# Performance work log

Hardware: AMD Instinct MI355X
Metric: run time of the kernel (lower is better)

## Reference

```python
import jax, jax.numpy as jnp
import numpy as np

N = 50000      # nodes
E = 800000     # edges
IN = 256       # in_dim
H = 3          # num_heads
C = 64         # hidden_dim (per head)
D = H * C      # per-layer width = 192
OUT = 64       # out_dim
EPS_BN = 1e-5


def _gat_layer(h, W, att_src, att_dst, bias, src, dst):
    """PyG GATConv (concat=True, no self loops, eval/no dropout).
    h: [N, F_in], W: [F_in, H*C], att_src/att_dst: [H, C], bias: [H*C]."""
    x = (h @ W).reshape(-1, H, C)                       # [N, H, C]
    a_s = jnp.einsum('nhc,hc->nh', x, att_src)          # [N, H]
    a_d = jnp.einsum('nhc,hc->nh', x, att_dst)          # [N, H]
    e = jax.nn.leaky_relu(a_s[src] + a_d[dst], 0.2)     # [E, H]
    # segment softmax over incoming edges of each destination node
    m = jax.ops.segment_max(e, dst, num_segments=N)     # [N, H]
    m = jnp.where(jnp.isfinite(m), m, 0.0)
    w = jnp.exp(e - m[dst])                             # [E, H]
    den = jax.ops.segment_sum(w, dst, num_segments=N)   # [N, H]
    alpha = w / (den[dst] + 1e-16)                      # [E, H]
    out = jax.ops.segment_sum(x[src] * alpha[:, :, None], dst, num_segments=N)
    return out.reshape(-1, D) + bias                    # [N, H*C]


def _batchnorm(h, gamma, beta):
    mu = h.mean(0)
    var = h.var(0)
    return (h - mu) * jax.lax.rsqrt(var + EPS_BN) * gamma + beta


def setup_inputs() -> dict:
    key = jax.random.key(0)
    ks = jax.random.split(key, 16)
    s_in = 1.0 / np.sqrt(IN)
    s_d = 1.0 / np.sqrt(D)
    inp = {
        'x': jax.random.normal(ks[0], (N, IN), jnp.float32),
        'W1': jax.random.normal(ks[1], (IN, D), jnp.float32) * s_in,
        'att_src1': jax.random.normal(ks[2], (H, C), jnp.float32) * s_d,
        'att_dst1': jax.random.normal(ks[3], (H, C), jnp.float32) * s_d,
        'b1': jnp.zeros((D,), jnp.float32),
        'g1': jnp.ones((D,), jnp.float32),
        'beta1': jnp.zeros((D,), jnp.float32),
        'W2': jax.random.normal(ks[4], (D, D), jnp.float32) * s_d,
        'att_src2': jax.random.normal(ks[5], (H, C), jnp.float32) * s_d,
        'att_dst2': jax.random.normal(ks[6], (H, C), jnp.float32) * s_d,
        'b2': jnp.zeros((D,), jnp.float32),
        'g2': jnp.ones((D,), jnp.float32),
        'beta2': jnp.zeros((D,), jnp.float32),
        'Wf': jax.random.normal(ks[7], (D, OUT), jnp.float32) * s_d,
        'bf': jnp.zeros((OUT,), jnp.float32),
        'edge_index': jax.random.randint(ks[8], (2, E), 0, N, jnp.int64),
    }
    return inp


def reference(x, W1, att_src1, att_dst1, b1, g1, beta1,
              W2, att_src2, att_dst2, b2, g2, beta2,
              Wf, bf, edge_index):
    src, dst = edge_index[0], edge_index[1]
    h1 = _gat_layer(x, W1, att_src1, att_dst1, b1, src, dst)
    h1 = _batchnorm(jax.nn.relu(h1), g1, beta1)
    h2 = _gat_layer(h1, W2, att_src2, att_dst2, b2, src, dst)
    h2 = _batchnorm(jax.nn.relu(h2), g2, beta2)
    h_sum = h1 + h2
    return h_sum @ Wf + bf
```

## Files before the change

kernel.cpp:

```cpp
#include <hip/hip_runtime.h>

#define NN 50000
#define NE 800000
#define DIN 256
#define NH 3
#define HC 64
#define DD 192
#define DF 64
#define NB 196

typedef __attribute__((ext_vector_type(8))) short s8bf;
typedef __attribute__((ext_vector_type(8))) unsigned short u16x8;
typedef __attribute__((ext_vector_type(4))) float f32x4;

__device__ __forceinline__ unsigned short f2bf(float f) {
    unsigned u = __float_as_uint(f);
    unsigned r = u + 0x7fffu + ((u >> 16) & 1u);
    return (unsigned short)(r >> 16);
}
__device__ __forceinline__ float bf2f(unsigned short h) {
    return __uint_as_float(((unsigned)h) << 16);
}
__device__ __forceinline__ void split2(float f, unsigned short& h, unsigned short& l) {
    h = f2bf(f);
    l = f2bf(f - bf2f(h));
}
__device__ __forceinline__ float rl_f(float v, int j) {
    return __int_as_float(__builtin_amdgcn_readlane(__float_as_int(v), j));
}

#define W1G (DIN / 8 * DD)
#define W2G (DD / 8 * DD)
#define WFG (DD / 8 * DF)
__global__ __launch_bounds__(256)
void wsplit_all(const float* __restrict__ W1, const float* __restrict__ W2,
                const float* __restrict__ Wf,
                unsigned short* __restrict__ W1hT, unsigned short* __restrict__ W1lT,
                unsigned short* __restrict__ W2hT, unsigned short* __restrict__ W2lT,
                unsigned short* __restrict__ WfhT, unsigned short* __restrict__ WflT) {
    int idx = blockIdx.x * 256 + threadIdx.x;
    const float* W; unsigned short *Wh, *Wl; int K, D, base;
    if (idx < W1G)                  { W = W1; Wh = W1hT; Wl = W1lT; K = DIN; D = DD; base = idx; }
    else if (idx < W1G + W2G)       { W = W2; Wh = W2hT; Wl = W2lT; K = DD;  D = DD; base = idx - W1G; }
    else if (idx < W1G + W2G + WFG) { W = Wf; Wh = WfhT; Wl = WflT; K = DD;  D = DF; base = idx - W1G - W2G; }
    else return;
    int kb = base / D, d = base - kb * D;
    u16x8 hv, lv;
#pragma unroll
    for (int q = 0; q < 8; ++q) {
        unsigned short h, l;
        split2(W[(size_t)(kb * 8 + q) * D + d], h, l);
        hv[q] = h; lv[q] = l;
    }
    *(u16x8*)(Wh + (size_t)d * K + kb * 8) = hv;
    *(u16x8*)(Wl + (size_t)d * K + kb * 8) = lv;
}

__global__ void bn_fin(const float* __restrict__ s1, const float* __restrict__ s2,
                       const float* __restrict__ g, const float* __restrict__ beta,
                       float* __restrict__ scale, float* __restrict__ shift) {
    int j = threadIdx.x;
    const float invn = 1.0f / NN;
    float mu = s1[j] * invn;
    float var = s2[j] * invn - mu * mu;
    float sc = g[j] * rsqrtf(var + 1e-5f);
    scale[j] = sc;
    shift[j] = beta[j] - mu * sc;
}

template<int K, int DOUT, int MODE, bool DOTS>
__global__ __launch_bounds__(256)
void mfma_gemm(const float* __restrict__ A1, const float* __restrict__ A2,
               const float* __restrict__ bb1, const float* __restrict__ sc1,
               const float* __restrict__ sh1,
               const float* __restrict__ bb2, const float* __restrict__ sc2,
               const float* __restrict__ sh2,
               const unsigned short* __restrict__ BhT, const unsigned short* __restrict__ BlT,
               const float* __restrict__ att_s, const float* __restrict__ att_d,
               float4* __restrict__ as4o, float4* __restrict__ ad4o,
               const float* __restrict__ obias, float* __restrict__ Yf,
               unsigned short* __restrict__ Yb, int n) {
    constexpr int NT = DOUT / 64;
    __shared__ unsigned short AH[2][512][8];
    __shared__ float sdots[DOTS ? 4 : 1][64][6];

    const int tid = threadIdx.x;
    const int wave = tid >> 6, lane = tid & 63;
    const int r = lane & 15, kg = lane >> 4;
    const int row0 = blockIdx.x * 64;
    const int col0 = wave * (DOUT / 4);

    auto stage = [&](int buf, int k0) {
#pragma unroll
        for (int half = 0; half < 2; ++half) {
            int slot = tid + half * 256;
            int row = slot >> 3, kb8 = slot & 7;
            int grow = min(row0 + row, n - 1);
            int j = k0 + kb8 * 8;
            const float* ap = A1 + (size_t)grow * K + j;
            float v[8];
            *(float4*)&v[0] = *(const float4*)ap;
            *(float4*)&v[4] = *(const float4*)(ap + 4);
            if constexpr (MODE >= 1) {
#pragma unroll
                for (int q = 0; q < 8; ++q)
                    v[q] = fmaxf(v[q] + bb1[j + q], 0.f) * sc1[j + q] + sh1[j + q];
            }
            if constexpr (MODE == 2) {
                const float* ap2 = A2 + (size_t)grow * K + j;
                float u[8];
                *(float4*)&u[0] = *(const float4*)ap2;
                *(float4*)&u[4] = *(const float4*)(ap2 + 4);
#pragma unroll
                for (int q = 0; q < 8; ++q)
                    v[q] += fmaxf(u[q] + bb2[j + q], 0.f) * sc2[j + q] + sh2[j + q];
            }
            u16x8 hv;
#pragma unroll
            for (int q = 0; q < 8; ++q)
                hv[q] = f2bf(v[q]);
            int sw = (row << 3) | (kb8 ^ (row & 7));
            *(u16x8*)&AH[buf][sw][0] = hv;
        }
    };

    int boff[NT];
#pragma unroll
    for (int t = 0; t < NT; ++t)
        boff[t] = (col0 + t * 16 + r) * K + kg * 8;

    f32x4 acc[4][NT] = {};

    stage(0, 0);
    __syncthreads();

    for (int k0 = 0; k0 < K; k0 += 64) {
        const int buf = (k0 >> 6) & 1;
        if (k0 + 64 < K) stage(buf ^ 1, k0 + 64);
#pragma unroll
        for (int s = 0; s < 2; ++s) {
            s8bf bh[NT], bl[NT];
#pragma unroll
            for (int t = 0; t < NT; ++t) {
                bh[t] = *(const s8bf*)(BhT + boff[t] + k0 + s * 32);
                bl[t] = *(const s8bf*)(BlT + boff[t] + k0 + s * 32);
            }
            s8bf ah[4];
#pragma unroll
            for (int g = 0; g < 4; ++g) {
                int row = g * 16 + r;
                int sw = (row << 3) | ((s * 4 + kg) ^ (row & 7));
                ah[g] = *(const s8bf*)&AH[buf][sw][0];
            }
#pragma unroll
            for (int g = 0; g < 4; ++g)
#pragma unroll
                for (int t = 0; t < NT; ++t) {
                    acc[g][t] = __builtin_amdgcn_mfma_f32_16x16x32_bf16(ah[g], bh[t], acc[g][t], 0, 0, 0);
                    acc[g][t] = __builtin_amdgcn_mfma_f32_16x16x32_bf16(ah[g], bl[t], acc[g][t], 0, 0, 0);
                }
        }
        __syncthreads();
    }

#pragma unroll
    for (int t = 0; t < NT; ++t) {
        int col = col0 + t * 16 + r;
        float b = (MODE == 2) ? obias[col] : 0.f;
#pragma unroll
        for (int g = 0; g < 4; ++g) {
#pragma unroll
            for (int rr = 0; rr < 4; ++rr) {
                int row = row0 + g * 16 + kg * 4 + rr;
                if (row < n) {
                    if constexpr (MODE == 2)
                        Yf[(size_t)row * DOUT + col] = acc[g][t][rr] + b;
                    else
                        Yb[(size_t)row * DOUT + col] = f2bf(acc[g][t][rr]);
                }
            }
        }
    }

    if constexpr (DOTS) {
        float asv[NT], adv[NT];
        int headt[NT];
#pragma unroll
        for (int t = 0; t < NT; ++t) {
            int col = col0 + t * 16 + r;
            asv[t] = att_s[col];
            adv[t] = att_d[col];
            headt[t] = (col0 + t * 16) >> 6;
        }
#pragma unroll
        for (int g = 0; g < 4; ++g) {
#pragma unroll
            for (int rr = 0; rr < 4; ++rr) {
                float rs0 = 0.f, rs1 = 0.f, rs2 = 0.f;
                float rd0 = 0.f, rd1 = 0.f, rd2 = 0.f;
#pragma unroll
                for (int t = 0; t < NT; ++t) {
                    float v = acc[g][t][rr];
                    float s = v * asv[t], dd = v * adv[t];
                    if (headt[t] == 0)      { rs0 += s; rd0 += dd; }
                    else if (headt[t] == 1) { rs1 += s; rd1 += dd; }
                    else                    { rs2 += s; rd2 += dd; }
                }
#pragma unroll
                for (int m = 1; m < 16; m <<= 1) {
                    rs0 += __shfl_xor(rs0, m); rs1 += __shfl_xor(rs1, m); rs2 += __shfl_xor(rs2, m);
                    rd0 += __shfl_xor(rd0, m); rd1 += __shfl_xor(rd1, m); rd2 += __shfl_xor(rd2, m);
                }
                if (r == 0) {
                    int row = g * 16 + kg * 4 + rr;
                    sdots[wave][row][0] = rs0; sdots[wave][row][1] = rs1; sdots[wave][row][2] = rs2;
                    sdots[wave][row][3] = rd0; sdots[wave][row][4] = rd1; sdots[wave][row][5] = rd2;
                }
            }
        }
        __syncthreads();
        if (tid < 64) {
            int row = row0 + tid;
            if (row < n) {
                float s0 = 0.f, s1 = 0.f, s2 = 0.f, d0 = 0.f, d1 = 0.f, d2 = 0.f;
#pragma unroll
                for (int w = 0; w < 4; ++w) {
                    s0 += sdots[w][tid][0]; s1 += sdots[w][tid][1]; s2 += sdots[w][tid][2];
                    d0 += sdots[w][tid][3]; d1 += sdots[w][tid][4]; d2 += sdots[w][tid][5];
                }
                as4o[row] = make_float4(s0, s1, s2, 0.f);
                ad4o[row] = make_float4(d0, d1, d2, 0.f);
            }
        }
    }
}

__global__ void hist_kernel(const int* __restrict__ dst, int* __restrict__ deg, int ne) {
    int e = blockIdx.x * blockDim.x + threadIdx.x;
    if (e < ne) atomicAdd(&deg[dst[e]], 1);
}

__global__ __launch_bounds__(256)
void blocksum_kernel(const int* __restrict__ deg, int* __restrict__ bsum) {
    int i = blockIdx.x * 256 + threadIdx.x;
    int v = (i < NN) ? deg[i] : 0;
#pragma unroll
    for (int off = 32; off; off >>= 1) v += __shfl_down(v, off);
    __shared__ int ws[4];
    if ((threadIdx.x & 63) == 0) ws[threadIdx.x >> 6] = v;
    __syncthreads();
    if (threadIdx.x == 0) bsum[blockIdx.x] = ws[0] + ws[1] + ws[2] + ws[3];
}

__global__ __launch_bounds__(256)
void scan_bsums(const int* __restrict__ bsum, int* __restrict__ boff,
                int* __restrict__ rowptr) {
    __shared__ int s[256];
    int t = threadIdx.x;
    int v = (t < NB) ? bsum[t] : 0;
    s[t] = v;
    __syncthreads();
    for (int off = 1; off < 256; off <<= 1) {
        int u = (t >= off) ? s[t - off] : 0;
        __syncthreads();
        s[t] += u;
        __syncthreads();
    }
    if (t < NB) boff[t] = s[t] - v;
    if (t == 255) rowptr[NN] = s[255];
}

__global__ __launch_bounds__(256)
void expand_kernel(const int* __restrict__ deg, const int* __restrict__ boff,
                   int* __restrict__ rowptr, int* __restrict__ cursor) {
    __shared__ int s[256];
    int t = threadIdx.x;
    int i = blockIdx.x * 256 + t;
    int v = (i < NN) ? deg[i] : 0;
    s[t] = v;
    __syncthreads();
    for (int off = 1; off < 256; off <<= 1) {
        int u = (t >= off) ? s[t - off] : 0;
        __syncthreads();
        s[t] += u;
        __syncthreads();
    }
    if (i < NN) {
        int excl = s[t] - v + boff[blockIdx.x];
        rowptr[i] = excl;
        cursor[i] = excl;
    }
}

__global__ void scatter_kernel(const int* __restrict__ src, const int* __restrict__ dst,
                               int* __restrict__ cursor, int* __restrict__ csr_src, int ne) {
    int e = blockIdx.x * blockDim.x + threadIdx.x;
    if (e >= ne) return;
    int d = dst[e];
    int pos = atomicAdd(&cursor[d], 1);
    csr_src[pos] = src[e];
}

__global__ __launch_bounds__(256)
void gat_gather(const unsigned short* __restrict__ xf,
                const float4* __restrict__ as4, const float4* __restrict__ ad4,
                const int* __restrict__ rowptr, const int* __restrict__ csr_src,
                float* __restrict__ outp) {
    int d = blockIdx.x * 4 + (threadIdx.x >> 6);
    if (d >= NN) return;
    const int lane = threadIdx.x & 63;
    const int beg = rowptr[d], end = rowptr[d + 1];
    const float4 adv = ad4[d];

    float a0 = 0.f, a1 = 0.f, a2 = 0.f;
    float den0 = 0.f, den1 = 0.f, den2 = 0.f;

    for (int base = beg; base < end; base += 64) {
        const int nb = min(64, end - base);
        int sl = 0;
        float w0 = 0.f, w1 = 0.f, w2 = 0.f;
        if (lane < nb) {
            sl = csr_src[base + lane];
            float4 av = as4[sl];
            float e0 = av.x + adv.x;
            float e1 = av.y + adv.y;
            float e2 = av.z + adv.z;
            e0 = e0 > 0.f ? e0 : 0.2f * e0;
            e1 = e1 > 0.f ? e1 : 0.2f * e1;
            e2 = e2 > 0.f ? e2 : 0.2f * e2;
            w0 = __expf(e0); w1 = __expf(e1); w2 = __expf(e2);
        }
        float r0 = w0, r1 = w1, r2 = w2;
#pragma unroll
        for (int off = 1; off < 64; off <<= 1) {
            r0 += __shfl_xor(r0, off);
            r1 += __shfl_xor(r1, off);
            r2 += __shfl_xor(r2, off);
        }
        den0 += r0; den1 += r1; den2 += r2;

        int j = 0;
        for (; j + 8 <= nb; j += 8) {
            const unsigned short* xp[8];
            float uw0[8], uw1[8], uw2[8];
#pragma unroll
            for (int k = 0; k < 8; ++k) {
                int s = __builtin_amdgcn_readlane(sl, j + k);
                xp[k] = xf + (size_t)s * DD;
                uw0[k] = rl_f(w0, j + k);
                uw1[k] = rl_f(w1, j + k);
                uw2[k] = rl_f(w2, j + k);
            }
            unsigned short f0[8], f1[8], f2[8];
#pragma unroll
            for (int k = 0; k < 8; ++k) {
                f0[k] = xp[k][lane];
                f1[k] = xp[k][64 + lane];
                f2[k] = xp[k][128 + lane];
            }
#pragma unroll
            for (int k = 0; k < 8; ++k) {
                a0 = fmaf(bf2f(f0[k]), uw0[k], a0);
                a1 = fmaf(bf2f(f1[k]), uw1[k], a1);
                a2 = fmaf(bf2f(f2[k]), uw2[k], a2);
            }
        }
        for (; j < nb; ++j) {
            int s = __builtin_amdgcn_readlane(sl, j);
            float u0 = rl_f(w0, j), u1 = rl_f(w1, j), u2 = rl_f(w2, j);
            const unsigned short* xp = xf + (size_t)s * DD;
            a0 = fmaf(bf2f(xp[lane]),       u0, a0);
            a1 = fmaf(bf2f(xp[64 + lane]),  u1, a1);
            a2 = fmaf(bf2f(xp[128 + lane]), u2, a2);
        }
    }
    size_t o = (size_t)d * DD + lane;
    outp[o]       = a0 / (den0 + 1e-16f);
    outp[o + 64]  = a1 / (den1 + 1e-16f);
    outp[o + 128] = a2 / (den2 + 1e-16f);
}

__global__ __launch_bounds__(192)
void bn_stats(const float* __restrict__ hbuf, const float* __restrict__ bias,
              float* __restrict__ s1, float* __restrict__ s2, int n) {
    int j = threadIdx.x;
    float b = bias[j];
    int r0 = blockIdx.x * 64;
    int r1 = min(r0 + 64, n);
    float a = 0.f, q = 0.f;
    for (int r = r0; r < r1; ++r) {
        float v = hbuf[(size_t)r * DD + j] + b;
        v = fmaxf(v, 0.f);
        a += v; q += v * v;
    }
    atomicAdd(&s1[j], a);
    atomicAdd(&s2[j], q);
}

extern "C" void kernel_launch(void* const* d_in, const int* in_sizes, int n_in,
                              void* d_out, int out_size, void* d_ws, size_t ws_size,
                              hipStream_t stream) {
    const float* x   = (const float*)d_in[0];
    const float* W1  = (const float*)d_in[1];
    const float* as1 = (const float*)d_in[2];
    const float* ad1 = (const float*)d_in[3];
    const float* b1  = (const float*)d_in[4];
    const float* g1  = (const float*)d_in[5];
    const float* be1 = (const float*)d_in[6];
    const float* W2  = (const float*)d_in[7];
    const float* as2 = (const float*)d_in[8];
    const float* ad2 = (const float*)d_in[9];
    const float* b2  = (const float*)d_in[10];
    const float* g2  = (const float*)d_in[11];
    const float* be2 = (const float*)d_in[12];
    const float* Wf  = (const float*)d_in[13];
    const float* bf  = (const float*)d_in[14];
    const int*   ei  = (const int*)d_in[15];
    const int* src = ei;
    const int* dst = ei + NE;
    float* out = (float*)d_out;

    float* ws = (float*)d_ws;
    float* CB1 = ws;
    float* CB2 = CB1 + (size_t)NN * DD;
    float4* AS4 = (float4*)(CB2 + (size_t)NN * DD);
    float4* AD4 = AS4 + NN;
    int* DEG   = (int*)(AD4 + NN);
    float* S1a = (float*)(DEG + NN);
    float* S2a = S1a + DD;
    float* S1b = S2a + DD;
    float* S2b = S1b + DD;
    float* SC1 = S2b + DD;
    float* SH1 = SC1 + DD;
    float* SC2 = SH1 + DD;
    float* SH2 = SC2 + DD;
    int* ROWPTR = (int*)(SH2 + DD);
    int* CURSOR = ROWPTR + NN + 1;
    int* BSUM   = CURSOR + NN;
    int* BOFF   = BSUM + NB;
    int* CSRS   = BOFF + NB;
    unsigned short* R    = (unsigned short*)(CSRS + NE);
    unsigned short* Abf  = R;
    unsigned short* W1hT = Abf + (size_t)NN * DD;
    unsigned short* W1lT = W1hT + DIN * DD;
    unsigned short* W2hT = W1lT + DIN * DD;
    unsigned short* W2lT = W2hT + DD * DD;
    unsigned short* WfhT = W2lT + DD * DD;
    unsigned short* WflT = WfhT + DD * DF;

    const int edge_grid = (NE + 255) / 256;
    const int gemm_grid = (NN + 63) / 64;
    const int gat_grid  = (NN + 3) / 4;
    const int bns_grid  = (NN + 63) / 64;
    const int wsp_grid  = (W1G + W2G + WFG + 255) / 256;

    hipMemsetAsync(DEG, 0, (size_t)NN * 4 + 4 * DD * 4, stream);

    hist_kernel<<<edge_grid, 256, 0, stream>>>(dst, DEG, NE);
    blocksum_kernel<<<NB, 256, 0, stream>>>(DEG, BSUM);
    scan_bsums<<<1, 256, 0, stream>>>(BSUM, BOFF, ROWPTR);
    expand_kernel<<<NB, 256, 0, stream>>>(DEG, BOFF, ROWPTR, CURSOR);
    scatter_kernel<<<edge_grid, 256, 0, stream>>>(src, dst, CURSOR, CSRS, NE);

    wsplit_all<<<wsp_grid, 256, 0, stream>>>(W1, W2, Wf, W1hT, W1lT, W2hT, W2lT, WfhT, WflT);

    mfma_gemm<DIN, DD, 0, true><<<gemm_grid, 256, 0, stream>>>(
        x, nullptr,
        nullptr, nullptr, nullptr,
        nullptr, nullptr, nullptr,
        W1hT, W1lT, as1, ad1, AS4, AD4, nullptr, nullptr, Abf, NN);
    gat_gather<<<gat_grid, 256, 0, stream>>>(Abf, AS4, AD4, ROWPTR, CSRS, CB1);
    bn_stats<<<bns_grid, 192, 0, stream>>>(CB1, b1, S1a, S2a, NN);
    bn_fin<<<1, DD, 0, stream>>>(S1a, S2a, g1, be1, SC1, SH1);

    mfma_gemm<DD, DD, 1, true><<<gemm_grid, 256, 0, stream>>>(
        CB1, nullptr,
        b1, SC1, SH1,
        nullptr, nullptr, nullptr,
        W2hT, W2lT, as2, ad2, AS4, AD4, nullptr, nullptr, Abf, NN);
    gat_gather<<<gat_grid, 256, 0, stream>>>(Abf, AS4, AD4, ROWPTR, CSRS, CB2);
    bn_stats<<<bns_grid, 192, 0, stream>>>(CB2, b2, S1b, S2b, NN);
    bn_fin<<<1, DD, 0, stream>>>(S1b, S2b, g2, be2, SC2, SH2);

    mfma_gemm<DD, DF, 2, false><<<gemm_grid, 256, 0, stream>>>(
        CB1, CB2,
        b1, SC1, SH1,
        b2, SC2, SH2,
        WfhT, WflT, nullptr, nullptr, nullptr, nullptr, bf, out, nullptr, NN);
}
```

Measured before the change: 417.4 us.

## Stage full-K A tile into LDS once instead of double-buffered K chunks

The GEMM kernel now loads and converts the whole 64-row by K-column A tile into shared memory in one pass, followed by a single barrier. The MFMA loop then runs over K in 32-wide steps with no per-chunk synchronization. This removes the per-iteration barriers and the double-buffer bookkeeping. In exchange it loses the overlap between global loads and MFMA work, and LDS use grows to 32KB for K=256, which may lower occupancy.

Measured after the change: 417.2 us. No clear change (-0.0%).

```diff
diff --git a/kernel.cpp b/kernel.cpp
--- a/kernel.cpp
+++ b/kernel.cpp
@@ -81,7 +81,8 @@
                const float* __restrict__ obias, float* __restrict__ Yf,
                unsigned short* __restrict__ Yb, int n) {
     constexpr int NT = DOUT / 64;
-    __shared__ unsigned short AH[2][512][8];
+    constexpr int KB8 = K / 8;
+    __shared__ unsigned short AH[64 * KB8 * 8];
     __shared__ float sdots[DOTS ? 4 : 1][64][6];
 
     const int tid = threadIdx.x;
@@ -90,39 +91,36 @@
     const int row0 = blockIdx.x * 64;
     const int col0 = wave * (DOUT / 4);
 
-    auto stage = [&](int buf, int k0) {
-#pragma unroll
-        for (int half = 0; half < 2; ++half) {
-            int slot = tid + half * 256;
-            int row = slot >> 3, kb8 = slot & 7;
-            int grow = min(row0 + row, n - 1);
-            int j = k0 + kb8 * 8;
-            const float* ap = A1 + (size_t)grow * K + j;
-            float v[8];
-            *(float4*)&v[0] = *(const float4*)ap;
-            *(float4*)&v[4] = *(const float4*)(ap + 4);
-            if constexpr (MODE >= 1) {
-#pragma unroll
-                for (int q = 0; q < 8; ++q)
-                    v[q] = fmaxf(v[q] + bb1[j + q], 0.f) * sc1[j + q] + sh1[j + q];
-            }
-            if constexpr (MODE == 2) {
-                const float* ap2 = A2 + (size_t)grow * K + j;
-                float u[8];
-                *(float4*)&u[0] = *(const float4*)ap2;
-                *(float4*)&u[4] = *(const float4*)(ap2 + 4);
-#pragma unroll
-                for (int q = 0; q < 8; ++q)
-                    v[q] += fmaxf(u[q] + bb2[j + q], 0.f) * sc2[j + q] + sh2[j + q];
-            }
-            u16x8 hv;
+    for (int idx = tid; idx < 64 * KB8; idx += 256) {
+        int row = idx / KB8, kb = idx - row * KB8;
+        int grow = min(row0 + row, n - 1);
+        int j = kb * 8;
+        const float* ap = A1 + (size_t)grow * K + j;
+        float v[8];
+        *(float4*)&v[0] = *(const float4*)ap;
+        *(float4*)&v[4] = *(const float4*)(ap + 4);
+        if constexpr (MODE >= 1) {
 #pragma unroll
             for (int q = 0; q < 8; ++q)
-                hv[q] = f2bf(v[q]);
-            int sw = (row << 3) | (kb8 ^ (row & 7));
-            *(u16x8*)&AH[buf][sw][0] = hv;
-        }
-    };
+                v[q] = fmaxf(v[q] + bb1[j + q], 0.f) * sc1[j + q] + sh1[j + q];
+        }
+        if constexpr (MODE == 2) {
+            const float* ap2 = A2 + (size_t)grow * K + j;
+            float u[8];
+            *(float4*)&u[0] = *(const float4*)ap2;
+            *(float4*)&u[4] = *(const float4*)(ap2 + 4);
+#pragma unroll
+            for (int q = 0; q < 8; ++q)
+                v[q] += fmaxf(u[q] + bb2[j + q], 0.f) * sc2[j + q] + sh2[j + q];
+        }
+        u16x8 hv;
+#pragma unroll
+        for (int q = 0; q < 8; ++q)
+            hv[q] = f2bf(v[q]);
+        int sw = kb ^ (row & 7);
+        *(u16x8*)&AH[(row * KB8 + sw) * 8] = hv;
+    }
+    __syncthreads();
 
     int boff[NT];
 #pragma unroll
@@ -131,36 +129,28 @@
 
     f32x4 acc[4][NT] = {};
 
-    stage(0, 0);
-    __syncthreads();
-
-    for (int k0 = 0; k0 < K; k0 += 64) {
-        const int buf = (k0 >> 6) & 1;
-        if (k0 + 64 < K) stage(buf ^ 1, k0 + 64);
-#pragma unroll
-        for (int s = 0; s < 2; ++s) {
-            s8bf bh[NT], bl[NT];
+    for (int k0 = 0; k0 < K; k0 += 32) {
+        s8bf bh[NT], bl[NT];
+#pragma unroll
+        for (int t = 0; t < NT; ++t) {
+            bh[t] = *(const s8bf*)(BhT + boff[t] + k0);
+            bl[t] = *(const s8bf*)(BlT + boff[t] + k0);
+        }
+        const int kb = k0 / 8 + kg;
+        s8bf ah[4];
+#pragma unroll
+        for (int g = 0; g < 4; ++g) {
+            int row = g * 16 + r;
+            int sw = kb ^ (row & 7);
+            ah[g] = *(const s8bf*)&AH[(row * KB8 + sw) * 8];
+        }
+#pragma unroll
+        for (int g = 0; g < 4; ++g)
 #pragma unroll
             for (int t = 0; t < NT; ++t) {
-                bh[t] = *(const s8bf*)(BhT + boff[t] + k0 + s * 32);
-                bl[t] = *(const s8bf*)(BlT + boff[t] + k0 + s * 32);
-            }
-            s8bf ah[4];
-#pragma unroll
-            for (int g = 0; g < 4; ++g) {
-                int row = g * 16 + r;
-                int sw = (row << 3) | ((s * 4 + kg) ^ (row & 7));
-                ah[g] = *(const s8bf*)&AH[buf][sw][0];
-            }
-#pragma unroll
-            for (int g = 0; g < 4; ++g)
-#pragma unroll
-                for (int t = 0; t < NT; ++t) {
-                    acc[g][t] = __builtin_amdgcn_mfma_f32_16x16x32_bf16(ah[g], bh[t], acc[g][t], 0, 0, 0);
-                    acc[g][t] = __builtin_amdgcn_mfma_f32_16x16x32_bf16(ah[g], bl[t], acc[g][t], 0, 0, 0);
-                }
-        }
-        __syncthreads();
+                acc[g][t] = __builtin_amdgcn_mfma_f32_16x16x32_bf16(ah[g], bh[t], acc[g][t], 0, 0, 0);
+                acc[g][t] = __builtin_amdgcn_mfma_f32_16x16x32_bf16(ah[g], bl[t], acc[g][t], 0, 0, 0);
+            }
     }
 
 #pragma unroll
```
